# Kernel tuning notes

Measured on AMD Instinct MI355X. Metric: run time of the kernel, lower is better.

## Reference

```python
import jax, jax.numpy as jnp
import numpy as np

N_NODES = 50000
N_EDGES = 800000
D_IN = 512
D_HID = 64
D_OUT = 40


def setup_inputs() -> dict:
    key = jax.random.key(0)
    ks = jax.random.split(key, 8)
    x = jax.random.normal(ks[0], (N_NODES, D_IN), dtype=jnp.float32)
    edge_index = jax.random.randint(ks[1], (2, N_EDGES), 0, N_NODES, dtype=jnp.int32)
    w_mul = jax.random.uniform(ks[2], (N_EDGES,), dtype=jnp.float32)
    s1 = 1.0 / np.sqrt(D_IN)
    s2 = 1.0 / np.sqrt(D_HID)
    W1 = jax.random.uniform(ks[3], (D_IN, D_HID), minval=-s1, maxval=s1, dtype=jnp.float32)
    b1 = jax.random.uniform(ks[4], (D_HID,), minval=-s1, maxval=s1, dtype=jnp.float32)
    W2 = jax.random.uniform(ks[5], (D_HID, D_OUT), minval=-s2, maxval=s2, dtype=jnp.float32)
    b2 = jax.random.uniform(ks[6], (D_OUT,), minval=-s2, maxval=s2, dtype=jnp.float32)
    return {"x": x, "edge_index": edge_index, "w_mul": w_mul,
            "W1": W1, "b1": b1, "W2": W2, "b2": b2}


def _conv(h, src, dst, w_mul, W, b, n_nodes):
    # linear transform, then gather-scale-scatter-add (PyG aggr='add')
    h = h @ W + b                      # [N, d_out]
    msg = w_mul[:, None] * h[src]      # [E, d_out] gather + scale
    return jax.ops.segment_sum(msg, dst, num_segments=n_nodes)  # scatter-add


def reference(x, edge_index, w_mul, W1, b1, W2, b2):
    n_nodes = x.shape[0]
    src, dst = edge_index[0], edge_index[1]  # flow: source_to_target
    h = _conv(x, src, dst, w_mul, W1, b1, n_nodes)
    h = jax.nn.relu(h)
    h = _conv(h, src, dst, w_mul, W2, b2, n_nodes)
    return jax.nn.log_softmax(h, axis=1)
```

## Files before the change

### kernel.cpp

```cpp
#include <hip/hip_runtime.h>
#include <math.h>

#define D_IN  512
#define D_HID 64
#define D_OUT 40
#define CAP   64

typedef __attribute__((ext_vector_type(8))) short bf16x8;
typedef __attribute__((ext_vector_type(4))) float f32x4;

static __device__ __forceinline__ unsigned short f2bf(float f) {
    unsigned u = __float_as_uint(f);
    return (unsigned short)((u + 0x7FFF + ((u >> 16) & 1)) >> 16);
}
static __device__ __forceinline__ float bf2f(unsigned short h) {
    return __uint_as_float(((unsigned)h) << 16);
}

__global__ __launch_bounds__(256)
void prep_all(int* __restrict__ cursor, const float* __restrict__ W1,
              unsigned short* __restrict__ w1T, const float* __restrict__ W2,
              unsigned short* __restrict__ w2T, int N) {
    const int i = blockIdx.x * blockDim.x + threadIdx.x;
    if (i < N) cursor[i] = 0;
    const int j = i - N;
    if (j >= 0 && j < D_IN * D_HID) {
        const int k = j >> 6, col = j & 63;
        w1T[col * D_IN + k] = f2bf(W1[j]);
    }
    const int l = j - D_IN * D_HID;
    if (l >= 0 && l < 48 * D_HID) {
        const int col = l >> 6, k = l & 63;
        w2T[l] = (col < D_OUT) ? f2bf(W2[k * D_OUT + col]) : 0;
    }
}

__global__ __launch_bounds__(256)
void fatA(const float* __restrict__ x, const unsigned short* __restrict__ w1T,
          const float* __restrict__ b1, unsigned short* __restrict__ h1,
          const int* __restrict__ src, const int* __restrict__ dstA,
          const float* __restrict__ wm, int* __restrict__ cursor,
          unsigned* __restrict__ edges, int E, int N, int g1Blocks) {
    __shared__ unsigned char lds[8192];
    const int t = threadIdx.x;

    if ((int)blockIdx.x < g1Blocks) {
        const int lane = t & 63;
        const int wv = t >> 6;
        const int nodeBase = blockIdx.x * 64;
        const int fr = lane & 15;
        const int fc = lane >> 4;

        int gn = nodeBase + wv * 16 + fr; if (gn >= N) gn = N - 1;
        const float* xrow = x + (size_t)gn * D_IN + fc * 8;

        f32x4 acc[4];
#pragma unroll
        for (int cg = 0; cg < 4; ++cg) acc[cg] = (f32x4){0.f, 0.f, 0.f, 0.f};

        for (int k0 = 0; k0 < D_IN; k0 += 64) {
            __syncthreads();
#pragma unroll
            for (int hh = 0; hh < 2; ++hh) {
                const int g = t + hh * 256;
                const int col = g >> 3, slot = g & 7;
                const uint4 p = *reinterpret_cast<const uint4*>(
                    w1T + (size_t)col * D_IN + k0 + slot * 8);
                *reinterpret_cast<uint4*>(
                    lds + col * 128 + ((slot << 4) ^ ((col & 7) << 4))) = p;
            }
            __syncthreads();

#pragma unroll
            for (int s = 0; s < 2; ++s) {
                const float4 a = *reinterpret_cast<const float4*>(xrow + k0 + s * 32);
                const float4 b = *reinterpret_cast<const float4*>(xrow + k0 + s * 32 + 4);
                uint4 p;
                p.x = (unsigned)f2bf(a.x) | ((unsigned)f2bf(a.y) << 16);
                p.y = (unsigned)f2bf(a.z) | ((unsigned)f2bf(a.w) << 16);
                p.z = (unsigned)f2bf(b.x) | ((unsigned)f2bf(b.y) << 16);
                p.w = (unsigned)f2bf(b.z) | ((unsigned)f2bf(b.w) << 16);
                const bf16x8 afrag = *reinterpret_cast<const bf16x8*>(&p);
                const int slot = s * 4 + fc;
#pragma unroll
                for (int cg = 0; cg < 4; ++cg) {
                    const int brow = cg * 16 + fr;
                    const bf16x8 bfrag = *reinterpret_cast<const bf16x8*>(
                        lds + brow * 128 + ((slot << 4) ^ ((brow & 7) << 4)));
                    acc[cg] = __builtin_amdgcn_mfma_f32_16x16x32_bf16(afrag, bfrag, acc[cg], 0, 0, 0);
                }
            }
        }

        const int rq = lane >> 4;
#pragma unroll
        for (int cg = 0; cg < 4; ++cg) {
            const int col = cg * 16 + fr;
            const float bb = b1[col];
#pragma unroll
            for (int r = 0; r < 4; ++r) {
                const int node = nodeBase + wv * 16 + rq * 4 + r;
                if (node < N)
                    h1[(size_t)node * D_HID + col] = f2bf(acc[cg][r] + bb);
            }
        }
    } else {
        const int slice = (N + 7) >> 3;
        const int lo = (blockIdx.x & 7) * slice;
        const int hi = min(N, lo + slice);
        const int localBid = blockIdx.x - g1Blocks;
        const int nChunk = (gridDim.x - g1Blocks) >> 3;
        const int per = (E + nChunk - 1) / nChunk;
        const int beg = (localBid >> 3) * per;
        const int end = min(E, beg + per);
        for (int e = beg + t; e < end; e += 256) {
            const int d = dstA[e];
            if (d >= lo && d < hi) {
                const int pos = atomicAdd(&cursor[d], 1);
                if (pos < CAP)
                    edges[(size_t)d * CAP + pos] =
                        ((unsigned)src[e] << 16) | (unsigned)f2bf(wm[e]);
            }
        }
    }
}

__global__ __launch_bounds__(256)
void fatB(const unsigned short* __restrict__ h1, const unsigned* __restrict__ edges,
          const int* __restrict__ count, const unsigned short* __restrict__ w2T,
          const float* __restrict__ b2, unsigned short* __restrict__ h2, int N) {
    __shared__ unsigned char lds[8192 + 6144];
    const int t = threadIdx.x;
    const int lane = t & 63;
    const int wv = t >> 6;
    const int nodeBase = blockIdx.x * 64;

    for (int g = t; g < 384; g += 256) {
        const int row = g >> 3, slot = g & 7;
        const uint4 p = *reinterpret_cast<const uint4*>(w2T + (size_t)row * D_HID + slot * 8);
        *reinterpret_cast<uint4*>(lds + 8192 + row * 128 + ((slot << 4) ^ ((row & 7) << 4))) = p;
    }

    {
        const int n0 = nodeBase + wv * 16;
        unsigned er = edges[(size_t)min(n0, N - 1) * CAP + lane];
        int cnt = (n0 < N) ? min(count[n0], CAP) : 0;
#pragma unroll 1
        for (int i = 0; i < 16; ++i) {
            const int r = wv * 16 + i;
            unsigned erN = 0; int cntN = 0;
            if (i < 15) {
                const int nn = nodeBase + r + 1;
                erN = edges[(size_t)min(nn, N - 1) * CAP + lane];
                cntN = (nn < N) ? min(count[nn], CAP) : 0;
            }
            float acc = 0.f;
            int j = 0;
            for (; j + 8 <= cnt; j += 8) {
                unsigned p[8];
#pragma unroll
                for (int u = 0; u < 8; ++u) p[u] = (unsigned)__shfl((int)er, j + u);
                float v[8];
#pragma unroll
                for (int u = 0; u < 8; ++u)
                    v[u] = bf2f(h1[(size_t)(p[u] >> 16) * D_HID + lane]);
#pragma unroll
                for (int u = 0; u < 8; ++u)
                    acc += bf2f((unsigned short)(p[u] & 0xffff)) * v[u];
            }
            for (; j < cnt; ++j) {
                const unsigned p0 = (unsigned)__shfl((int)er, j);
                acc += bf2f((unsigned short)(p0 & 0xffff)) *
                       bf2f(h1[(size_t)(p0 >> 16) * D_HID + lane]);
            }
            const unsigned short hv = f2bf(fmaxf(acc, 0.f));
            *reinterpret_cast<unsigned short*>(
                lds + r * 128 + (((lane >> 3) << 4) ^ ((r & 7) << 4)) + (lane & 7) * 2) = hv;
            er = erN; cnt = cntN;
        }
    }
    __syncthreads();

    f32x4 acc2[3];
#pragma unroll
    for (int cg = 0; cg < 3; ++cg) acc2[cg] = (f32x4){0.f, 0.f, 0.f, 0.f};

    const int fr = lane & 15;
    const int fc = lane >> 4;
#pragma unroll
    for (int s = 0; s < 2; ++s) {
        const int slot = s * 4 + fc;
        const int arow = wv * 16 + fr;
        const bf16x8 afrag = *reinterpret_cast<const bf16x8*>(
            lds + arow * 128 + ((slot << 4) ^ ((arow & 7) << 4)));
#pragma unroll
        for (int cg = 0; cg < 3; ++cg) {
            const int brow = cg * 16 + fr;
            const bf16x8 bfrag = *reinterpret_cast<const bf16x8*>(
                lds + 8192 + brow * 128 + ((slot << 4) ^ ((brow & 7) << 4)));
            acc2[cg] = __builtin_amdgcn_mfma_f32_16x16x32_bf16(afrag, bfrag, acc2[cg], 0, 0, 0);
        }
    }

    const int rq = lane >> 4;
#pragma unroll
    for (int cg = 0; cg < 3; ++cg) {
        const int col = cg * 16 + fr;
        if (col < D_OUT) {
            const float bb = b2[col];
#pragma unroll
            for (int r = 0; r < 4; ++r) {
                const int node = nodeBase + wv * 16 + rq * 4 + r;
                if (node < N)
                    h2[(size_t)node * D_OUT + col] = f2bf(acc2[cg][r] + bb);
            }
        }
    }
}

__global__ __launch_bounds__(256)
void agg40_lsm(const unsigned short* __restrict__ h2, const unsigned* __restrict__ edges,
               const int* __restrict__ count, float* __restrict__ out, int N) {
    const int lane = threadIdx.x & 63;
    const int col  = (lane < D_OUT) ? lane : 0;
    const int n = (blockIdx.x * blockDim.x + threadIdx.x) >> 6;
    if (n >= N) return;
    const unsigned er = edges[(size_t)n * CAP + lane];
    const int cnt = min(count[n], CAP);
    float acc = 0.f;
    int j = 0;
    for (; j + 8 <= cnt; j += 8) {
        unsigned p[8];
#pragma unroll
        for (int u = 0; u < 8; ++u) p[u] = (unsigned)__shfl((int)er, j + u);
        float v[8];
#pragma unroll
        for (int u = 0; u < 8; ++u) v[u] = bf2f(h2[(size_t)(p[u] >> 16) * D_OUT + col]);
#pragma unroll
        for (int u = 0; u < 8; ++u)
            acc += bf2f((unsigned short)(p[u] & 0xffff)) * v[u];
    }
    for (; j < cnt; ++j) {
        const unsigned p0 = (unsigned)__shfl((int)er, j);
        acc += bf2f((unsigned short)(p0 & 0xffff)) *
               bf2f(h2[(size_t)(p0 >> 16) * D_OUT + col]);
    }
    const float v = (lane < D_OUT) ? acc : -INFINITY;
    float m = v;
#pragma unroll
    for (int o = 32; o > 0; o >>= 1) m = fmaxf(m, __shfl_xor(m, o, 64));
    float s = (lane < D_OUT) ? __expf(v - m) : 0.f;
#pragma unroll
    for (int o = 32; o > 0; o >>= 1) s += __shfl_xor(s, o, 64);
    if (lane < D_OUT) out[(size_t)n * D_OUT + lane] = v - m - __logf(s);
}

extern "C" void kernel_launch(void* const* d_in, const int* in_sizes, int n_in,
                              void* d_out, int out_size, void* d_ws, size_t ws_size,
                              hipStream_t stream) {
    const float* x   = (const float*)d_in[0];
    const int*   ei  = (const int*)d_in[1];
    const float* wm  = (const float*)d_in[2];
    const float* W1  = (const float*)d_in[3];
    const float* b1  = (const float*)d_in[4];
    const float* W2  = (const float*)d_in[5];
    const float* b2  = (const float*)d_in[6];

    const int N = in_sizes[0] / D_IN;
    const int E = in_sizes[2];
    const int* srcIdx = ei;
    const int* dstIdx = ei + E;

    unsigned short* w1T  = (unsigned short*)d_ws;
    unsigned short* h1bf = w1T + (size_t)D_HID * D_IN;
    unsigned short* h2bf = h1bf + (size_t)N * D_HID;
    unsigned* edges      = (unsigned*)(h2bf + (size_t)N * D_HID);
    int*   cursor        = (int*)(edges + (size_t)N * CAP);
    unsigned short* w2T  = (unsigned short*)(cursor + N);
    float* out           = (float*)d_out;

    const int g1Blocks = (N + 63) / 64;
    const int scatterBlocks = 1024;
    const int prepWork = N + D_IN * D_HID + 48 * D_HID;

    prep_all<<<(prepWork + 255) / 256, 256, 0, stream>>>(cursor, W1, w1T, W2, w2T, N);
    fatA<<<g1Blocks + scatterBlocks, 256, 0, stream>>>(
        x, w1T, b1, h1bf, srcIdx, dstIdx, wm, cursor, edges, E, N, g1Blocks);
    fatB<<<g1Blocks, 256, 0, stream>>>(h1bf, edges, cursor, w2T, b2, h2bf, N);
    agg40_lsm<<<(N * 64 + 255) / 256, 256, 0, stream>>>(h2bf, edges, cursor, out, N);
}
```

Baseline: 139.7 us.

## Split fused GEMM/scatter kernel; stage full W1 in LDS once per block

The fused kernel that ran the first GEMM and the edge bucketing in one grid is split into two separate launches. The GEMM now loads all of W1^T (64KB) into LDS once and then runs the K loop with no further barriers. The scatter kernel gets 2048 blocks instead of 1024. This removes the per-k-step syncthreads and the shared-grid branching, but it gives up the concurrent overlap of GEMM and scatter, and 64KB of LDS per block limits occupancy.

```diff
diff --git a/kernel.cpp b/kernel.cpp
--- a/kernel.cpp
+++ b/kernel.cpp
@@ -36,91 +36,86 @@
 }
 
 __global__ __launch_bounds__(256)
-void fatA(const float* __restrict__ x, const unsigned short* __restrict__ w1T,
-          const float* __restrict__ b1, unsigned short* __restrict__ h1,
-          const int* __restrict__ src, const int* __restrict__ dstA,
-          const float* __restrict__ wm, int* __restrict__ cursor,
-          unsigned* __restrict__ edges, int E, int N, int g1Blocks) {
-    __shared__ unsigned char lds[8192];
+void scatter_cap(const int* __restrict__ src, const int* __restrict__ dstA,
+                 const float* __restrict__ wm, int* __restrict__ cursor,
+                 unsigned* __restrict__ edges, int E, int N) {
+    const int slice = (N + 7) >> 3;
+    const int lo = (blockIdx.x & 7) * slice;
+    const int hi = min(N, lo + slice);
+    const int nChunk = gridDim.x >> 3;
+    const int per = (E + nChunk - 1) / nChunk;
+    const int beg = (blockIdx.x >> 3) * per;
+    const int end = min(E, beg + per);
+    for (int e = beg + threadIdx.x; e < end; e += blockDim.x) {
+        const int d = dstA[e];
+        if (d >= lo && d < hi) {
+            const int pos = atomicAdd(&cursor[d], 1);
+            if (pos < CAP)
+                edges[(size_t)d * CAP + pos] =
+                    ((unsigned)src[e] << 16) | (unsigned)f2bf(wm[e]);
+        }
+    }
+}
+
+__global__ __launch_bounds__(256)
+void gemm1_mfma(const float* __restrict__ x, const unsigned short* __restrict__ w1T,
+                const float* __restrict__ b1, unsigned short* __restrict__ h1, int N) {
+    __shared__ unsigned char lds[65536];
     const int t = threadIdx.x;
-
-    if ((int)blockIdx.x < g1Blocks) {
-        const int lane = t & 63;
-        const int wv = t >> 6;
-        const int nodeBase = blockIdx.x * 64;
-        const int fr = lane & 15;
-        const int fc = lane >> 4;
-
-        int gn = nodeBase + wv * 16 + fr; if (gn >= N) gn = N - 1;
-        const float* xrow = x + (size_t)gn * D_IN + fc * 8;
-
-        f32x4 acc[4];
-#pragma unroll
-        for (int cg = 0; cg < 4; ++cg) acc[cg] = (f32x4){0.f, 0.f, 0.f, 0.f};
-
-        for (int k0 = 0; k0 < D_IN; k0 += 64) {
-            __syncthreads();
-#pragma unroll
-            for (int hh = 0; hh < 2; ++hh) {
-                const int g = t + hh * 256;
-                const int col = g >> 3, slot = g & 7;
-                const uint4 p = *reinterpret_cast<const uint4*>(
-                    w1T + (size_t)col * D_IN + k0 + slot * 8);
-                *reinterpret_cast<uint4*>(
-                    lds + col * 128 + ((slot << 4) ^ ((col & 7) << 4))) = p;
-            }
-            __syncthreads();
-
-#pragma unroll
-            for (int s = 0; s < 2; ++s) {
-                const float4 a = *reinterpret_cast<const float4*>(xrow + k0 + s * 32);
-                const float4 b = *reinterpret_cast<const float4*>(xrow + k0 + s * 32 + 4);
-                uint4 p;
-                p.x = (unsigned)f2bf(a.x) | ((unsigned)f2bf(a.y) << 16);
-                p.y = (unsigned)f2bf(a.z) | ((unsigned)f2bf(a.w) << 16);
-                p.z = (unsigned)f2bf(b.x) | ((unsigned)f2bf(b.y) << 16);
-                p.w = (unsigned)f2bf(b.z) | ((unsigned)f2bf(b.w) << 16);
-                const bf16x8 afrag = *reinterpret_cast<const bf16x8*>(&p);
-                const int slot = s * 4 + fc;
-#pragma unroll
-                for (int cg = 0; cg < 4; ++cg) {
-                    const int brow = cg * 16 + fr;
-                    const bf16x8 bfrag = *reinterpret_cast<const bf16x8*>(
-                        lds + brow * 128 + ((slot << 4) ^ ((brow & 7) << 4)));
-                    acc[cg] = __builtin_amdgcn_mfma_f32_16x16x32_bf16(afrag, bfrag, acc[cg], 0, 0, 0);
-                }
-            }
-        }
-
-        const int rq = lane >> 4;
-#pragma unroll
-        for (int cg = 0; cg < 4; ++cg) {
-            const int col = cg * 16 + fr;
-            const float bb = b1[col];
-#pragma unroll
-            for (int r = 0; r < 4; ++r) {
-                const int node = nodeBase + wv * 16 + rq * 4 + r;
-                if (node < N)
-                    h1[(size_t)node * D_HID + col] = f2bf(acc[cg][r] + bb);
-            }
-        }
-    } else {
-        const int slice = (N + 7) >> 3;
-        const int lo = (blockIdx.x & 7) * slice;
-        const int hi = min(N, lo + slice);
-        const int localBid = blockIdx.x - g1Blocks;
-        const int nChunk = (gridDim.x - g1Blocks) >> 3;
-        const int per = (E + nChunk - 1) / nChunk;
-        const int beg = (localBid >> 3) * per;
-        const int end = min(E, beg + per);
-        for (int e = beg + t; e < end; e += 256) {
-            const int d = dstA[e];
-            if (d >= lo && d < hi) {
-                const int pos = atomicAdd(&cursor[d], 1);
-                if (pos < CAP)
-                    edges[(size_t)d * CAP + pos] =
-                        ((unsigned)src[e] << 16) | (unsigned)f2bf(wm[e]);
-            }
+    const int lane = t & 63;
+    const int wv = t >> 6;
+    const int nodeBase = blockIdx.x * 64;
+    const int fr = lane & 15;
+    const int fc = lane >> 4;
+
+#pragma unroll
+    for (int g = t; g < 4096; g += 256) {
+        const int col = g >> 6, gs = g & 63;
+        const uint4 p = *reinterpret_cast<const uint4*>(w1T + (size_t)col * D_IN + gs * 8);
+        *reinterpret_cast<uint4*>(lds + col * 1024 + ((gs * 16) ^ ((col & 7) << 4))) = p;
+    }
+    __syncthreads();
+
+    int gn = nodeBase + wv * 16 + fr; if (gn >= N) gn = N - 1;
+    const float* xrow = x + (size_t)gn * D_IN + fc * 8;
+
+    f32x4 acc[4];
+#pragma unroll
+    for (int cg = 0; cg < 4; ++cg) acc[cg] = (f32x4){0.f, 0.f, 0.f, 0.f};
+
+#pragma unroll
+    for (int k0 = 0; k0 < D_IN; k0 += 64) {
+#pragma unroll
+        for (int s = 0; s < 2; ++s) {
+            const float4 a = *reinterpret_cast<const float4*>(xrow + k0 + s * 32);
+            const float4 b = *reinterpret_cast<const float4*>(xrow + k0 + s * 32 + 4);
+            uint4 p;
+            p.x = (unsigned)f2bf(a.x) | ((unsigned)f2bf(a.y) << 16);
+            p.y = (unsigned)f2bf(a.z) | ((unsigned)f2bf(a.w) << 16);
+            p.z = (unsigned)f2bf(b.x) | ((unsigned)f2bf(b.y) << 16);
+            p.w = (unsigned)f2bf(b.z) | ((unsigned)f2bf(b.w) << 16);
+            const bf16x8 afrag = *reinterpret_cast<const bf16x8*>(&p);
+            const int slot = s * 4 + fc;
+#pragma unroll
+            for (int cg = 0; cg < 4; ++cg) {
+                const int brow = cg * 16 + fr;
+                const bf16x8 bfrag = *reinterpret_cast<const bf16x8*>(
+                    lds + brow * 1024 + k0 * 2 + ((slot << 4) ^ ((brow & 7) << 4)));
+                acc[cg] = __builtin_amdgcn_mfma_f32_16x16x32_bf16(afrag, bfrag, acc[cg], 0, 0, 0);
+            }
+        }
+    }
+
+    const int rq = lane >> 4;
+#pragma unroll
+    for (int cg = 0; cg < 4; ++cg) {
+        const int col = cg * 16 + fr;
+        const float bb = b1[col];
+#pragma unroll
+        for (int r = 0; r < 4; ++r) {
+            const int node = nodeBase + wv * 16 + rq * 4 + r;
+            if (node < N)
+                h1[(size_t)node * D_HID + col] = f2bf(acc[cg][r] + bb);
         }
     }
 }
@@ -280,12 +275,11 @@
     float* out           = (float*)d_out;
 
     const int g1Blocks = (N + 63) / 64;
-    const int scatterBlocks = 1024;
     const int prepWork = N + D_IN * D_HID + 48 * D_HID;
 
     prep_all<<<(prepWork + 255) / 256, 256, 0, stream>>>(cursor, W1, w1T, W2, w2T, N);
-    fatA<<<g1Blocks + scatterBlocks, 256, 0, stream>>>(
-        x, w1T, b1, h1bf, srcIdx, dstIdx, wm, cursor, edges, E, N, g1Blocks);
+    gemm1_mfma<<<g1Blocks, 256, 0, stream>>>(x, w1T, b1, h1bf, N);
+    scatter_cap<<<2048, 256, 0, stream>>>(srcIdx, dstIdx, wm, cursor, edges, E, N);
     fatB<<<g1Blocks, 256, 0, stream>>>(h1bf, edges, cursor, w2T, b2, h2bf, N);
     agg40_lsm<<<(N * 64 + 255) / 256, 256, 0, stream>>>(h2bf, edges, cursor, out, N);
 }
```

Measured after the change: 151.9 us. +8.7%, slower.
